# Kernel tuning notes

Hardware: AMD Instinct MI355X
Metric: run time of the kernel (lower is better)

## Reference

```python
import jax, jax.numpy as jnp
import numpy as np

N_QUBITS = 14
HIDDEN = 14
BATCH = 2048
DIM = 2 ** N_QUBITS
CDT = jnp.complex64


def _cnot_perm(n, c, t):
    # permutation for CNOT(control=c, target=t); wire 0 = most significant bit
    idx = np.arange(2 ** n)
    cm = 1 << (n - 1 - c)
    tm = 1 << (n - 1 - t)
    return np.where((idx & cm) != 0, idx ^ tm, idx)


def _apply_1q(state, gate, w):
    # state: (B, 2^n); gate: (2,2) shared or (B,2,2) batched
    B = state.shape[0]
    L, R = 2 ** w, 2 ** (N_QUBITS - w - 1)
    s = state.reshape(B, L, 2, R)
    if gate.ndim == 2:
        s = jnp.einsum('ij,bljr->blir', gate, s)
    else:
        s = jnp.einsum('bij,bljr->blir', gate, s)
    return s.reshape(B, DIM)


def _apply_diag(state, d0, d1, w):
    # batched diagonal 1q gate diag(d0, d1); d0,d1: (B,) complex
    B = state.shape[0]
    L, R = 2 ** w, 2 ** (N_QUBITS - w - 1)
    d = jnp.stack([d0, d1], axis=-1)[:, None, :, None]  # (B,1,2,1)
    return (state.reshape(B, L, 2, R) * d).reshape(B, DIM)


_H = np.array([[1.0, 1.0], [1.0, -1.0]], dtype=np.complex64) / np.float32(np.sqrt(2.0))
_IDX = np.arange(DIM)
_SIGNS = np.stack(
    [1.0 - 2.0 * ((_IDX >> (N_QUBITS - 1 - w)) & 1) for w in range(HIDDEN)], axis=1
).astype(np.float32)  # (2^n, HIDDEN): Z eigenvalues per basis state per wire
_CNOT_PERMS = [
    _cnot_perm(N_QUBITS, c, (c + step) % N_QUBITS)
    for step in (1, 2)
    for c in range(N_QUBITS)
]


def _simulate(x, u3_params):
    B = x.shape[0]
    ry = jnp.arctan(x)        # (B, n) encoded RY angles
    rz = jnp.arctan(x * x)    # (B, n) encoded RZ angles
    state = jnp.zeros((B, DIM), dtype=CDT).at[:, 0].set(1.0)
    H = jnp.asarray(_H)
    # H layer
    for w in range(N_QUBITS):
        state = _apply_1q(state, H, w)
    # RY layer (batched angles)
    for w in range(N_QUBITS):
        th = ry[:, w] * 0.5
        c, s = jnp.cos(th).astype(CDT), jnp.sin(th).astype(CDT)
        g = jnp.stack([jnp.stack([c, -s], -1), jnp.stack([s, c], -1)], -2)  # (B,2,2)
        state = _apply_1q(state, g, w)
    # RZ layer (batched, diagonal)
    for w in range(N_QUBITS):
        th = rz[:, w] * 0.5
        e = jnp.exp(1j * th.astype(CDT))
        state = _apply_diag(state, jnp.conj(e), e, w)
    # CNOT ring step=1 then step=2 (pure index permutations)
    for perm in _CNOT_PERMS:
        state = state[:, perm]
    # U3 layer (learned, shared across batch)
    th, ph, lam = u3_params[:, 0], u3_params[:, 1], u3_params[:, 2]
    for w in range(N_QUBITS):
        t2 = th[w] * 0.5
        ct = jnp.cos(t2).astype(CDT)
        st = jnp.sin(t2).astype(CDT)
        el = jnp.exp(1j * lam[w].astype(CDT))
        ep = jnp.exp(1j * ph[w].astype(CDT))
        g = jnp.stack(
            [jnp.stack([ct, -el * st], -1), jnp.stack([ep * st, ep * el * ct], -1)], -2
        )  # (2,2)
        state = _apply_1q(state, g, w)
    # <Z_w> expectations for w in 0..HIDDEN-1
    probs = state.real ** 2 + state.imag ** 2  # (B, 2^n)
    return probs @ jnp.asarray(_SIGNS)         # (B, HIDDEN)


def setup_inputs() -> dict:
    key = jax.random.key(0)
    k1, k2 = jax.random.split(key)
    x = jax.random.normal(k1, (BATCH, N_QUBITS), dtype=jnp.float32)
    u3_params = jax.random.uniform(
        k2, (N_QUBITS, 3), dtype=jnp.float32, minval=0.0, maxval=2.0 * np.pi
    )
    return {"x": x, "u3_params": u3_params}


def reference(x, u3_params):
    return _simulate(x, u3_params)
```

## Files before the change

kernel.cpp:

```cpp
#include <hip/hip_runtime.h>

#define NQ 14

constexpr unsigned perm_step(int k, unsigned v) {
    const int step = (k < NQ) ? 1 : 2;
    const int c = k % NQ;
    const int t = (c + step) % NQ;
    const unsigned cm = 1u << (NQ - 1 - c);
    const unsigned tm = 1u << (NQ - 1 - t);
    return (v & cm) ? (v ^ tm) : v;
}

constexpr unsigned Qapply(unsigned v) {
    for (int k = 2 * NQ - 1; k >= 0; --k) v = perm_step(k, v);
    return v;
}
constexpr unsigned Qinvapply(unsigned v) {
    for (int k = 0; k < 2 * NQ; ++k) v = perm_step(k, v);
    return v;
}

struct MaskTab {
    unsigned f[NQ];
    unsigned m[NQ];
    float    sg[NQ];
};

constexpr MaskTab make_masks() {
    MaskTab T{};
    for (int w = 0; w < NQ; ++w) {
        T.f[w] = Qapply(1u << (NQ - 1 - w));
        unsigned mm = 0;
        for (int p = 0; p < NQ; ++p) {
            const unsigned qi = Qinvapply(1u << p);
            if ((qi >> (NQ - 1 - w)) & 1u) mm |= (1u << p);
        }
        T.m[w] = mm;
        unsigned kk = 0;
        const unsigned fm = T.f[w] & mm;
        for (int p = 0; p < NQ; ++p) kk += (fm >> p) & 1u;
        T.sg[w] = (((kk - 1u) / 2u) & 1u) ? -1.0f : 1.0f;
    }
    return T;
}

constexpr MaskTab TAB = make_masks();

__global__ __launch_bounds__(64)
void qulinear_expect_kernel(const float* __restrict__ x,
                            const float* __restrict__ u3,
                            float* __restrict__ out, int B)
{
    __shared__ float cth[NQ], scl[NQ], ssl[NQ];
    if (threadIdx.x < NQ) {
        const int w = threadIdx.x;
        const float th  = u3[3 * w + 0];
        const float lam = u3[3 * w + 2];
        float st, ct, sl, cl;
        sincosf(th, &st, &ct);
        sincosf(lam, &sl, &cl);
        cth[w] = ct;
        scl[w] = st * cl;
        ssl[w] = st * sl;
    }
    __syncthreads();

    const int b = blockIdx.x * blockDim.x + threadIdx.x;
    if (b >= B) return;

    float z[NQ], t[NQ], g[NQ];
#pragma unroll
    for (int v = 0; v < NQ; ++v) {
        const float xv = x[b * NQ + v];
        const float x2 = xv * xv;
        const float cy = rsqrtf(1.0f + x2);
        const float cz = rsqrtf(1.0f + x2 * x2);
        z[v] = -xv * cy;
        t[v] = cy * cz;
        g[v] = x2 * cy * cz;
    }

#pragma unroll
    for (int w = 0; w < NQ; ++w) {
        const unsigned fm = TAB.f[w];
        const unsigned mm = TAB.m[w];
        float P1 = 1.0f, P2 = 1.0f, P3 = 1.0f;
#pragma unroll
        for (int p = 0; p < NQ; ++p) {
            const int v = NQ - 1 - p;
            const bool inF = (fm >> p) & 1u;
            const bool inM = (mm >> p) & 1u;
            if (inM)            P1 *= z[v];
            if (inF)            P2 *= t[v];
            if (inF && inM)     P3 *= g[v];
            else if (inF)       P3 *= t[v];
            else if (inM)       P3 *= z[v];
        }
        out[b * NQ + w] = cth[w] * P1 - scl[w] * P2 + TAB.sg[w] * ssl[w] * P3;
    }
}

extern "C" void kernel_launch(void* const* d_in, const int* in_sizes, int n_in,
                              void* d_out, int out_size, void* d_ws, size_t ws_size,
                              hipStream_t stream) {
    const float* x  = (const float*)d_in[0];
    const float* u3 = (const float*)d_in[1];
    float* out = (float*)d_out;
    const int B = in_sizes[0] / NQ;
    const int block = 64;
    const int grid = (B + block - 1) / block;
    qulinear_expect_kernel<<<grid, block, 0, stream>>>(x, u3, out, B);
}
```

Measured before the change: 9.868 us.

## Stage input and output through padded LDS with float4 coalesced accesses

```diff
diff --git a/kernel.cpp b/kernel.cpp
--- a/kernel.cpp
+++ b/kernel.cpp
@@ -1,6 +1,8 @@
 #include <hip/hip_runtime.h>
 
 #define NQ 14
+#define BLK 128
+#define PAD 15
 
 constexpr unsigned perm_step(int k, unsigned v) {
     const int step = (k < NQ) ? 1 : 2;
@@ -46,12 +48,17 @@
 
 constexpr MaskTab TAB = make_masks();
 
-__global__ __launch_bounds__(64)
+__global__ __launch_bounds__(BLK)
 void qulinear_expect_kernel(const float* __restrict__ x,
                             const float* __restrict__ u3,
                             float* __restrict__ out, int B)
 {
+    __shared__ float lds[BLK * PAD];
     __shared__ float cth[NQ], scl[NQ], ssl[NQ];
+
+    const int total = B * NQ;
+    const int base_e = blockIdx.x * (BLK * NQ);
+
     if (threadIdx.x < NQ) {
         const int w = threadIdx.x;
         const float th  = u3[3 * w + 0];
@@ -63,15 +70,25 @@
         scl[w] = st * cl;
         ssl[w] = st * sl;
     }
+
+    for (int i = threadIdx.x; i < (BLK * NQ) / 4; i += BLK) {
+        const int e = i * 4;
+        float4 v4 = make_float4(0.f, 0.f, 0.f, 0.f);
+        if (base_e + e + 3 < total)
+            v4 = *(const float4*)(x + base_e + e);
+#pragma unroll
+        for (int j = 0; j < 4; ++j) {
+            const int ee = e + j;
+            lds[(ee / NQ) * PAD + (ee % NQ)] = (&v4.x)[j];
+        }
+    }
     __syncthreads();
 
-    const int b = blockIdx.x * blockDim.x + threadIdx.x;
-    if (b >= B) return;
-
+    const int r = threadIdx.x;
     float z[NQ], t[NQ], g[NQ];
 #pragma unroll
     for (int v = 0; v < NQ; ++v) {
-        const float xv = x[b * NQ + v];
+        const float xv = lds[r * PAD + v];
         const float x2 = xv * xv;
         const float cy = rsqrtf(1.0f + x2);
         const float cz = rsqrtf(1.0f + x2 * x2);
@@ -80,23 +97,44 @@
         g[v] = x2 * cy * cz;
     }
 
+    float outv[NQ];
 #pragma unroll
     for (int w = 0; w < NQ; ++w) {
         const unsigned fm = TAB.f[w];
         const unsigned mm = TAB.m[w];
-        float P1 = 1.0f, P2 = 1.0f, P3 = 1.0f;
+        float P1a = 1.f, P1b = 1.f, P2a = 1.f, P2b = 1.f, P3a = 1.f, P3b = 1.f;
 #pragma unroll
         for (int p = 0; p < NQ; ++p) {
             const int v = NQ - 1 - p;
             const bool inF = (fm >> p) & 1u;
             const bool inM = (mm >> p) & 1u;
-            if (inM)            P1 *= z[v];
-            if (inF)            P2 *= t[v];
-            if (inF && inM)     P3 *= g[v];
-            else if (inF)       P3 *= t[v];
-            else if (inM)       P3 *= z[v];
+            const bool alt = p & 1;
+            if (inM)          { if (alt) P1b *= z[v]; else P1a *= z[v]; }
+            if (inF)          { if (alt) P2b *= t[v]; else P2a *= t[v]; }
+            if (inF && inM)   { if (alt) P3b *= g[v]; else P3a *= g[v]; }
+            else if (inF)     { if (alt) P3b *= t[v]; else P3a *= t[v]; }
+            else if (inM)     { if (alt) P3b *= z[v]; else P3a *= z[v]; }
         }
-        out[b * NQ + w] = cth[w] * P1 - scl[w] * P2 + TAB.sg[w] * ssl[w] * P3;
+        outv[w] = cth[w] * (P1a * P1b) - scl[w] * (P2a * P2b)
+                + TAB.sg[w] * ssl[w] * (P3a * P3b);
+    }
+    __syncthreads();
+
+#pragma unroll
+    for (int w = 0; w < NQ; ++w) lds[r * PAD + w] = outv[w];
+    __syncthreads();
+
+    for (int i = threadIdx.x; i < (BLK * NQ) / 4; i += BLK) {
+        const int e = i * 4;
+        if (base_e + e + 3 < total) {
+            float4 v4;
+#pragma unroll
+            for (int j = 0; j < 4; ++j) {
+                const int ee = e + j;
+                (&v4.x)[j] = lds[(ee / NQ) * PAD + (ee % NQ)];
+            }
+            *(float4*)(out + base_e + e) = v4;
+        }
     }
 }
 
@@ -107,7 +145,6 @@
     const float* u3 = (const float*)d_in[1];
     float* out = (float*)d_out;
     const int B = in_sizes[0] / NQ;
-    const int block = 64;
-    const int grid = (B + block - 1) / block;
-    qulinear_expect_kernel<<<grid, block, 0, stream>>>(x, u3, out, B);
+    const int grid = (B + BLK - 1) / BLK;
+    qulinear_expect_kernel<<<grid, BLK, 0, stream>>>(x, u3, out, B);
 }
```

Result: no change. 9.753 us (-1.2%).
